# Optimization experiments

Measured on AMD Instinct MI355X. Metric: run time of the kernel, lower is better.

Reference implementation:

```python
import jax, jax.numpy as jnp
import numpy as np

N_EMBD = 1024
N_HEAD = 16
HEAD_SIZE = N_EMBD // N_HEAD  # 64

def setup_inputs() -> dict:
    key = jax.random.key(0)
    ks = jax.random.split(key, 6)
    B, T, C, H, S = 2, 2048, N_EMBD, N_HEAD, HEAD_SIZE
    sc = 1.0 / np.sqrt(C)
    x = jax.random.normal(ks[0], (B, T, C), dtype=jnp.float32)
    # stacked per-head projection weights (no bias), [H, C, S]
    Wq = jax.random.normal(ks[1], (H, C, S), dtype=jnp.float32) * sc
    Wk = jax.random.normal(ks[2], (H, C, S), dtype=jnp.float32) * sc
    Wv = jax.random.normal(ks[3], (H, C, S), dtype=jnp.float32) * sc
    Wp = jax.random.normal(ks[4], (C, C), dtype=jnp.float32) * sc
    bp = jax.random.normal(ks[5], (C,), dtype=jnp.float32) * 0.01
    return {"x": x, "Wq": Wq, "Wk": Wk, "Wv": Wv, "Wp": Wp, "bp": bp}

def reference(x, Wq, Wk, Wv, Wp, bp):
    # Eval-mode forward (dropout = identity), default non-flash path.
    B, T, C = x.shape
    H, _, S = Wq.shape
    q = jnp.einsum('btc,hcs->bhts', x, Wq)
    k = jnp.einsum('btc,hcs->bhts', x, Wk)
    v = jnp.einsum('btc,hcs->bhts', x, Wv)
    att = jnp.einsum('bhts,bhus->bhtu', q, k) * (1.0 / np.sqrt(S))
    causal = jnp.tril(jnp.ones((T, T), dtype=bool))
    att = jnp.where(causal[None, None], att, -jnp.inf)
    att = jax.nn.softmax(att, axis=-1)
    y = jnp.einsum('bhtu,bhus->bhts', att, v)
    # concat heads along feature dim (head-major), then output projection
    y = y.transpose(0, 2, 1, 3).reshape(B, T, H * S)
    return y @ Wp.T + bp
```

## Files before the change

### kernel.cpp

```cpp
#include <hip/hip_runtime.h>
#include <hip/hip_bf16.h>
#include <cmath>

typedef __attribute__((ext_vector_type(8))) short bf16x8;
typedef __attribute__((ext_vector_type(4))) float f32x4;
typedef __attribute__((ext_vector_type(16))) float f32x16;

__device__ __forceinline__ unsigned short f2bf(float f) {
    union { float f; unsigned int i; } c; c.f = f;
    unsigned int i = c.i;
    unsigned int r = i + 0x7FFF + ((i >> 16) & 1);
    return (unsigned short)(r >> 16);
}

__device__ __forceinline__ float fast_exp2(float x) {
    float r;
    asm("v_exp_f32 %0, %1" : "=v"(r) : "v"(x));
    return r;
}

__device__ __forceinline__ void gload_lds16(const unsigned short* g, unsigned short* l) {
    __builtin_amdgcn_global_load_lds((const __attribute__((address_space(1))) unsigned int*)g,
                                     (__attribute__((address_space(3))) unsigned int*)l, 16, 0, 0);
}

__global__ void k_cvt_all(const float* __restrict__ x, const float* __restrict__ Wp,
                          const float* __restrict__ Wq, const float* __restrict__ Wk,
                          const float* __restrict__ Wv,
                          unsigned short* __restrict__ x_bf, unsigned short* __restrict__ Wp_bf,
                          unsigned short* __restrict__ Wt) {
    __shared__ unsigned short lt[64][72];
    int bid = blockIdx.x;
    int t = threadIdx.x;
    if (bid < 5120) {
        const float* src = (bid < 4096) ? x : Wp;
        unsigned short* dst = (bid < 4096) ? x_bf : Wp_bf;
        int i = ((bid < 4096) ? bid : (bid - 4096)) * 256 + t;
        float4 v = reinterpret_cast<const float4*>(src)[i];
        ushort4 o;
        o.x = f2bf(v.x); o.y = f2bf(v.y); o.z = f2bf(v.z); o.w = f2bf(v.w);
        reinterpret_cast<ushort4*>(dst)[i] = o;
        return;
    }
    int sub = bid - 5120;
    int ct  = sub & 15;
    int h   = (sub >> 4) & 15;
    int sec = sub >> 8;
    const float* W = (sec == 0) ? Wq : ((sec == 1) ? Wk : Wv);
    float sc = (sec == 0) ? 0.1803368801f : 1.0f;
    #pragma unroll
    for (int q = 0; q < 4; q++) {
        int id = t + q * 256;
        int c  = id >> 4;
        int s4 = (id & 15) * 4;
        float4 v = *reinterpret_cast<const float4*>(&W[((size_t)(h * 1024) + (ct * 64 + c)) * 64 + s4]);
        lt[s4 + 0][c] = f2bf(v.x * sc);
        lt[s4 + 1][c] = f2bf(v.y * sc);
        lt[s4 + 2][c] = f2bf(v.z * sc);
        lt[s4 + 3][c] = f2bf(v.w * sc);
    }
    __syncthreads();
    #pragma unroll
    for (int q = 0; q < 2; q++) {
        int id = t + q * 256;
        int s  = id >> 3;
        int c8 = (id & 7) * 8;
        bf16x8 val = *reinterpret_cast<const bf16x8*>(&lt[s][c8]);
        int n = sec * 1024 + h * 64 + s;
        *reinterpret_cast<bf16x8*>(&Wt[(size_t)n * 1024 + ct * 64 + c8]) = val;
    }
}

__launch_bounds__(256, 3)
__global__ void k_gemm_qkv(const unsigned short* __restrict__ x_bf,
                           const unsigned short* __restrict__ Wt,
                           unsigned short* __restrict__ q_nat,
                           unsigned short* __restrict__ k_nat,
                           unsigned short* __restrict__ vT) {
    __shared__ unsigned short Asm[3][128][32];
    __shared__ unsigned short Bsm[3][128][32];
    const int K = 1024;
    int cpx = gridDim.x >> 3;
    int bid = (blockIdx.x & 7) * cpx + (blockIdx.x >> 3);
    bool isV = (bid >= 512);
    const unsigned short* A;
    const unsigned short* Bt;
    int m0, n0;
    if (!isV) {
        n0 = (bid & 15) << 7;
        m0 = (bid >> 4) << 7;
        A = x_bf; Bt = Wt;
    } else {
        int vb = bid - 512;
        n0 = (vb & 31) << 7;
        m0 = (vb >> 5) << 7;
        A = Wt + (size_t)2048 * 1024;
        Bt = x_bf;
    }
    int t = threadIdx.x;
    int lane = t & 63, w = t >> 6;
    int wr = w >> 1, wc = w & 1;
    int l15 = lane & 15, lg = lane >> 4;
    int srow = lane >> 2;
    int scol = ((lane & 3) ^ ((lane >> 3) & 3)) << 3;

    f32x4 acc[4][4];
    #pragma unroll
    for (int i = 0; i < 4; i++)
        #pragma unroll
        for (int j = 0; j < 4; j++) acc[i][j] = (f32x4){0.f, 0.f, 0.f, 0.f};

    auto STAGE = [&](int kt, int buf) {
        #pragma unroll
        for (int q = 0; q < 2; q++) {
            int rb = q * 64 + w * 16;
            int row = rb + srow;
            gload_lds16(&A[(size_t)(m0 + row) * K + kt + scol], &Asm[buf][rb][0]);
            gload_lds16(&Bt[(size_t)(n0 + row) * K + kt + scol], &Bsm[buf][rb][0]);
        }
    };

    const int NT = K >> 5;
    STAGE(0, 0);
    STAGE(32, 1);
    asm volatile("s_waitcnt vmcnt(4)" ::: "memory");
    __builtin_amdgcn_s_barrier();
    int cur = 0;

    for (int tt = 0; tt < NT; tt++) {
        bool more = (tt + 2 < NT);
        if (more) {
            int sbuf = cur + 2; if (sbuf >= 3) sbuf -= 3;
            STAGE((tt + 2) << 5, sbuf);
        }

        bf16x8 af[4], bfr[4];
        int xg = (l15 >> 1) & 3;
        #pragma unroll
        for (int mi = 0; mi < 4; mi++) {
            int row = wr * 64 + mi * 16 + l15;
            af[mi] = *reinterpret_cast<const bf16x8*>((const char*)&Asm[cur][row][0] + ((lg ^ xg) << 4));
        }
        #pragma unroll
        for (int nj = 0; nj < 4; nj++) {
            int row = wc * 64 + nj * 16 + l15;
            bfr[nj] = *reinterpret_cast<const bf16x8*>((const char*)&Bsm[cur][row][0] + ((lg ^ xg) << 4));
        }
        asm volatile("s_waitcnt lgkmcnt(0)" ::: "memory");
        __builtin_amdgcn_sched_barrier(0);
        __builtin_amdgcn_s_setprio(1);
        #pragma unroll
        for (int mi = 0; mi < 4; mi++)
            #pragma unroll
            for (int nj = 0; nj < 4; nj++)
                acc[mi][nj] = __builtin_amdgcn_mfma_f32_16x16x32_bf16(af[mi], bfr[nj], acc[mi][nj], 0, 0, 0);
        __builtin_amdgcn_s_setprio(0);

        if (more) {
            asm volatile("s_waitcnt vmcnt(4)" ::: "memory");
        } else {
            asm volatile("s_waitcnt vmcnt(0)" ::: "memory");
        }
        __builtin_amdgcn_s_barrier();
        cur = (cur == 2) ? 0 : cur + 1;
    }

    unsigned short* qkdst = nullptr;
    int noff = 0;
    if (!isV) { qkdst = (n0 < 1024) ? q_nat : k_nat; noff = (n0 < 1024) ? 0 : 1024; }
    #pragma unroll
    for (int mi = 0; mi < 4; mi++) {
        #pragma unroll
        for (int nj = 0; nj < 4; nj++) {
            #pragma unroll
            for (int r = 0; r < 4; r++) {
                int m = m0 + wr * 64 + mi * 16 + lg * 4 + r;
                int n = n0 + wc * 64 + nj * 16 + l15;
                float v = acc[mi][nj][r];
                if (!isV) {
                    qkdst[(size_t)m * 1024 + (n - noff)] = f2bf(v);
                } else {
                    int bb = n >> 11, ttn = n & 2047;
                    int hh = m >> 6, ss = m & 63;
                    vT[(((size_t)(bb * 16 + hh)) * 64 + ss) * 2048 + ttn] = f2bf(v);
                }
            }
        }
    }
}

__launch_bounds__(512, 4)
__global__ void k_attn(const unsigned short* __restrict__ q_nat,
                       const unsigned short* __restrict__ k_nat,
                       const unsigned short* __restrict__ vT,
                       unsigned short* __restrict__ y_bf) {
    __shared__ __align__(16) unsigned short SM[2][2][128][64];
    __shared__ float clB[128];
    const int T = 2048, H = 16;
    int bid = blockIdx.x;
    int bh = bid & 31;
    int g  = bid >> 5;
    int p  = (g < 8) ? (15 - g) : (g - 8);
    int h = bh & 15, b = bh >> 4;
    int t = threadIdx.x;
    int lane = t & 63, w = t >> 6;
    int pr = w >> 2, rg = w & 3;
    int l31 = lane & 31, hi = lane >> 5;
    int q0 = p << 7;
    int warp_q0 = q0 + rg * 32;
    int qg = warp_q0 + l31;

    const unsigned short* kbase = k_nat + (size_t)(b * T) * 1024 + h * 64;
    const unsigned short* vbase = vT + ((size_t)(b * H + h) * 64) * 2048;

    int sxor = ((lane & 7) ^ (lane >> 3)) << 3;

    auto STAGE = [&](int jt) {
        #pragma unroll
        for (int r = 0; r < 4; r++) {
            int rb = r * 32 + rg * 8;
            int grow = rb + (lane >> 3);
            gload_lds16(kbase + (size_t)(jt * 128 + grow) * 1024 + sxor, &SM[0][pr][rb][0]);
            gload_lds16(vbase + (size_t)(grow & 63) * 2048 + jt * 128 + (grow >> 6) * 64 + sxor,
                        &SM[1][pr][rb][0]);
        }
    };

    bf16x8 qf[4];
    #pragma unroll
    for (int tt = 0; tt < 4; tt++)
        qf[tt] = *reinterpret_cast<const bf16x8*>(
            q_nat + (size_t)(b * T + qg) * 1024 + h * 64 + tt * 16 + hi * 8);

    bf16x8 ones;
    #pragma unroll
    for (int z = 0; z < 8; z++) ones[z] = (short)0x3F80;

    f32x16 acc0, acc1, lacc;
    #pragma unroll
    for (int r = 0; r < 16; r++) { acc0[r] = 0.f; acc1[r] = 0.f; lacc[r] = 0.f; }

    if (pr == 0) STAGE(0);
    __syncthreads();

    for (int k = 0; k <= p; k++) {
        bool iCompute = (pr == (k & 1));
        if (!iCompute) {
            if (k + 1 <= p) STAGE(k + 1);
        } else {
            int rsw = (l31 & 7) << 4;
            #pragma unroll
            for (int jj = 0; jj < 2; jj++) {
                const char* kb = (const char*)&SM[0][pr][jj * 64][0];
                const char* vb = (const char*)&SM[1][pr][jj * 64][0];
                int j64 = 2 * k + jj;

                f32x16 s0, s1;
                #pragma unroll
                for (int r = 0; r < 16; r++) { s0[r] = 0.f; s1[r] = 0.f; }
                __builtin_amdgcn_s_setprio(1);
                #pragma unroll
                for (int tt = 0; tt < 4; tt++) {
                    int cb = (tt * 32 + hi * 16) ^ rsw;
                    bf16x8 kf0 = *reinterpret_cast<const bf16x8*>(kb + l31 * 128 + cb);
                    bf16x8 kf1 = *reinterpret_cast<const bf16x8*>(kb + (32 + l31) * 128 + cb);
                    s0 = __builtin_amdgcn_mfma_f32_32x32x16_bf16(kf0, qf[tt], s0, 0, 0, 0);
                    s1 = __builtin_amdgcn_mfma_f32_32x32x16_bf16(kf1, qf[tt], s1, 0, 0, 0);
                }
                __builtin_amdgcn_s_setprio(0);

                if (j64 * 64 + 63 > warp_q0) {
                    #pragma unroll
                    for (int r = 0; r < 16; r++) {
                        int kvr = (r & 3) + 8 * (r >> 2) + 4 * hi + j64 * 64;
                        if (kvr > qg) s0[r] = -INFINITY;
                        if (kvr + 32 > qg) s1[r] = -INFINITY;
                    }
                }

                #pragma unroll
                for (int r = 0; r < 16; r++) {
                    s0[r] = fast_exp2(s0[r]);
                    s1[r] = fast_exp2(s1[r]);
                }

                unsigned int c[16];
                #pragma unroll
                for (int i2 = 0; i2 < 8; i2++) {
                    asm("v_cvt_pk_bf16_f32 %0, %1, %2" : "=v"(c[i2]) : "v"(s0[2 * i2]), "v"(s0[2 * i2 + 1]));
                    asm("v_cvt_pk_bf16_f32 %0, %1, %2" : "=v"(c[8 + i2]) : "v"(s1[2 * i2]), "v"(s1[2 * i2 + 1]));
                }
                bf16x8 pa[4];
                #pragma unroll
                for (int ks = 0; ks < 4; ks++) {
                    unsigned int clo0 = c[ks * 4 + 0], clo1 = c[ks * 4 + 1];
                    unsigned int chi0 = c[ks * 4 + 2], chi1 = c[ks * 4 + 3];
                    unsigned int pl0 = (unsigned int)__shfl_xor((int)clo0, 32, 64);
                    unsigned int pl1 = (unsigned int)__shfl_xor((int)clo1, 32, 64);
                    unsigned int ph0 = (unsigned int)__shfl_xor((int)chi0, 32, 64);
                    unsigned int ph1 = (unsigned int)__shfl_xor((int)chi1, 32, 64);
                    union { unsigned int u[4]; bf16x8 v; } fr;
                    fr.u[0] = hi ? ph0 : clo0;
                    fr.u[1] = hi ? ph1 : clo1;
                    fr.u[2] = hi ? chi0 : pl0;
                    fr.u[3] = hi ? chi1 : pl1;
                    pa[ks] = fr.v;
                }

                __builtin_amdgcn_s_setprio(1);
                #pragma unroll
                for (int ks = 0; ks < 4; ks++) {
                    int cb = (ks * 32 + hi * 16) ^ rsw;
                    bf16x8 v0 = *reinterpret_cast<const bf16x8*>(vb + l31 * 128 + cb);
                    bf16x8 v1 = *reinterpret_cast<const bf16x8*>(vb + (32 + l31) * 128 + cb);
                    acc0 = __builtin_amdgcn_mfma_f32_32x32x16_bf16(pa[ks], v0, acc0, 0, 0, 0);
                    acc1 = __builtin_amdgcn_mfma_f32_32x32x16_bf16(pa[ks], v1, acc1, 0, 0, 0);
                    lacc = __builtin_amdgcn_mfma_f32_32x32x16_bf16(pa[ks], ones, lacc, 0, 0, 0);
                }
                __builtin_amdgcn_s_setprio(0);
            }
        }

        __syncthreads();
    }

    float* Ocomb = (float*)&SM[0][0][0][0];
    if (pr == 1) {
        #pragma unroll
        for (int r = 0; r < 16; r++) {
            int qr = (r & 3) + 8 * (r >> 2) + 4 * hi;
            int rr = rg * 32 + qr;
            Ocomb[rr * 64 + l31] = acc0[r];
            Ocomb[rr * 64 + 32 + l31] = acc1[r];
            if (l31 == 0) clB[rr] = lacc[r];
        }
    }
    __syncthreads();
    if (pr == 0) {
        #pragma unroll
        for (int r = 0; r < 16; r++) {
            int qr = (r & 3) + 8 * (r >> 2) + 4 * hi;
            int rr = rg * 32 + qr;
            float lt2 = lacc[r] + clB[rr];
            float dv = 1.0f / lt2;
            float o0 = acc0[r] + Ocomb[rr * 64 + l31];
            float o1 = acc1[r] + Ocomb[rr * 64 + 32 + l31];
            size_t row = (size_t)(b * T + q0 + rr) * 1024 + h * 64;
            y_bf[row + l31] = f2bf(o0 * dv);
            y_bf[row + 32 + l31] = f2bf(o1 * dv);
        }
    }
}

__launch_bounds__(256, 2)
__global__ void k_gemm_proj(const unsigned short* __restrict__ A,
                            const unsigned short* __restrict__ Bt,
                            float* __restrict__ out, const float* __restrict__ bp) {
    __shared__ unsigned short Asm[2][128][64];
    __shared__ unsigned short Bsm[2][64][64];
    const int K = 1024, nb = 16;
    int cpx = gridDim.x >> 3;
    int bid = (blockIdx.x & 7) * cpx + (blockIdx.x >> 3);
    int n0 = (bid % nb) << 6;
    int m0 = (bid / nb) << 7;
    int t = threadIdx.x;
    int lane = t & 63, w = t >> 6;
    int wr = w >> 1, wc = w & 1;
    int l15 = lane & 15, lg = lane >> 4;
    int sr = lane >> 3;
    int scol = ((lane & 7) ^ sr) << 3;

    f32x4 acc[4][2];
    #pragma unroll
    for (int i = 0; i < 4; i++)
        #pragma unroll
        for (int j = 0; j < 2; j++) acc[i][j] = (f32x4){0.f, 0.f, 0.f, 0.f};

    auto STAGE = [&](int kt, int buf) {
        #pragma unroll
        for (int q = 0; q < 4; q++) {
            int rb = q * 32 + w * 8;
            gload_lds16(&A[(size_t)(m0 + rb + sr) * K + kt + scol], &Asm[buf][rb][0]);
        }
        #pragma unroll
        for (int q = 0; q < 2; q++) {
            int rb = q * 32 + w * 8;
            gload_lds16(&Bt[(size_t)(n0 + rb + sr) * K + kt + scol], &Bsm[buf][rb][0]);
        }
    };

    const int NT = K >> 6;
    STAGE(0, 0);
    asm volatile("s_waitcnt vmcnt(0)" ::: "memory");
    __builtin_amdgcn_s_barrier();
    int cur = 0;

    for (int tt = 0; tt < NT; tt++) {
        if (tt + 1 < NT) STAGE((tt + 1) << 6, cur ^ 1);
        bf16x8 af[4][2], bfr[2][2];
        int x15 = (l15 & 7) << 3;
        #pragma unroll
        for (int mi = 0; mi < 4; mi++) {
            int row = wr * 64 + mi * 16 + l15;
            af[mi][0] = *reinterpret_cast<const bf16x8*>(&Asm[cur][row][(lg * 8) ^ x15]);
            af[mi][1] = *reinterpret_cast<const bf16x8*>(&Asm[cur][row][(32 + lg * 8) ^ x15]);
        }
        #pragma unroll
        for (int nj = 0; nj < 2; nj++) {
            int row = wc * 32 + nj * 16 + l15;
            bfr[nj][0] = *reinterpret_cast<const bf16x8*>(&Bsm[cur][row][(lg * 8) ^ x15]);
            bfr[nj][1] = *reinterpret_cast<const bf16x8*>(&Bsm[cur][row][(32 + lg * 8) ^ x15]);
        }
        asm volatile("s_waitcnt lgkmcnt(0)" ::: "memory");
        __builtin_amdgcn_sched_barrier(0);
        __builtin_amdgcn_s_setprio(1);
        #pragma unroll
        for (int mi = 0; mi < 4; mi++)
            #pragma unroll
            for (int nj = 0; nj < 2; nj++) {
                acc[mi][nj] = __builtin_amdgcn_mfma_f32_16x16x32_bf16(af[mi][0], bfr[nj][0], acc[mi][nj], 0, 0, 0);
                acc[mi][nj] = __builtin_amdgcn_mfma_f32_16x16x32_bf16(af[mi][1], bfr[nj][1], acc[mi][nj], 0, 0, 0);
            }
        __builtin_amdgcn_s_setprio(0);
        asm volatile("s_waitcnt vmcnt(0)" ::: "memory");
        __builtin_amdgcn_s_barrier();
        cur ^= 1;
    }

    #pragma unroll
    for (int mi = 0; mi < 4; mi++)
        #pragma unroll
        for (int nj = 0; nj < 2; nj++)
            #pragma unroll
            for (int r = 0; r < 4; r++) {
                int m = m0 + wr * 64 + mi * 16 + lg * 4 + r;
                int n = n0 + wc * 32 + nj * 16 + l15;
                out[(size_t)m * 1024 + n] = acc[mi][nj][r] + bp[n];
            }
}

extern "C" void kernel_launch(void* const* d_in, const int* in_sizes, int n_in,
                              void* d_out, int out_size, void* d_ws, size_t ws_size,
                              hipStream_t stream) {
    const float* x  = (const float*)d_in[0];
    const float* Wq = (const float*)d_in[1];
    const float* Wk = (const float*)d_in[2];
    const float* Wv = (const float*)d_in[3];
    const float* Wp = (const float*)d_in[4];
    const float* bp = (const float*)d_in[5];
    float* out = (float*)d_out;

    char* ws = (char*)d_ws;
    unsigned short* x_bf  = (unsigned short*)(ws);
    unsigned short* Wt    = (unsigned short*)(ws + ((size_t)8  << 20));
    unsigned short* Wp_bf = (unsigned short*)(ws + ((size_t)14 << 20));
    unsigned short* q_nat = (unsigned short*)(ws + ((size_t)16 << 20));
    unsigned short* k_nat = (unsigned short*)(ws + ((size_t)24 << 20));
    unsigned short* vT    = (unsigned short*)(ws + ((size_t)32 << 20));
    unsigned short* y_bf  = (unsigned short*)(ws + ((size_t)40 << 20));

    k_cvt_all<<<5888, 256, 0, stream>>>(x, Wp, Wq, Wk, Wv, x_bf, Wp_bf, Wt);
    k_gemm_qkv<<<768, 256, 0, stream>>>(x_bf, Wt, q_nat, k_nat, vT);
    k_attn<<<512, 512, 0, stream>>>(q_nat, k_nat, vT, y_bf);
    k_gemm_proj<<<512, 256, 0, stream>>>(y_bf, Wp_bf, out, bp);
}
```

Baseline: 101.2 us.

## Replace ping-pong warp groups with double-buffered all-warp prefetch in attention

Previously half the warps loaded the next K/V tile while the other half computed both 64-row halves of the current tile. Now every warp issues part of the prefetch into an alternate buffer, then each warp-group computes one 64-key half of the current tile, so all warps do MFMA work every iteration. The launch-bounds occupancy hint drops from 4 to 2 blocks, which gives the compiler more registers per thread but may lower occupancy. The shared layout is reinterpreted as two buffers, and the final combine that reuses SM is unchanged.

```diff
diff --git a/kernel.cpp b/kernel.cpp
--- a/kernel.cpp
+++ b/kernel.cpp
@@ -189,7 +189,7 @@
     }
 }
 
-__launch_bounds__(512, 4)
+__launch_bounds__(512, 2)
 __global__ void k_attn(const unsigned short* __restrict__ q_nat,
                        const unsigned short* __restrict__ k_nat,
                        const unsigned short* __restrict__ vT,
@@ -215,14 +215,15 @@
 
     int sxor = ((lane & 7) ^ (lane >> 3)) << 3;
 
-    auto STAGE = [&](int jt) {
-        #pragma unroll
-        for (int r = 0; r < 4; r++) {
-            int rb = r * 32 + rg * 8;
+    auto STAGE = [&](int jt, int buf) {
+        #pragma unroll
+        for (int q = 0; q < 2; q++) {
+            int rb = w * 16 + q * 8;
             int grow = rb + (lane >> 3);
-            gload_lds16(kbase + (size_t)(jt * 128 + grow) * 1024 + sxor, &SM[0][pr][rb][0]);
+            gload_lds16(kbase + (size_t)(jt * 128 + grow) * 1024 + sxor,
+                        (unsigned short*)&SM[buf][0][0][0] + rb * 64);
             gload_lds16(vbase + (size_t)(grow & 63) * 2048 + jt * 128 + (grow >> 6) * 64 + sxor,
-                        &SM[1][pr][rb][0]);
+                        (unsigned short*)&SM[buf][1][0][0] + rb * 64);
         }
     };
 
@@ -240,88 +241,84 @@
     #pragma unroll
     for (int r = 0; r < 16; r++) { acc0[r] = 0.f; acc1[r] = 0.f; lacc[r] = 0.f; }
 
-    if (pr == 0) STAGE(0);
+    STAGE(0, 0);
     __syncthreads();
+    int buf = 0;
 
     for (int k = 0; k <= p; k++) {
-        bool iCompute = (pr == (k & 1));
-        if (!iCompute) {
-            if (k + 1 <= p) STAGE(k + 1);
-        } else {
-            int rsw = (l31 & 7) << 4;
+        if (k < p) STAGE(k + 1, buf ^ 1);
+
+        const char* kb = (const char*)&SM[buf][0][pr * 64][0];
+        const char* vb = (const char*)&SM[buf][1][pr * 64][0];
+        int rsw = (l31 & 7) << 4;
+        int j64 = 2 * k + pr;
+
+        f32x16 s0, s1;
+        #pragma unroll
+        for (int r = 0; r < 16; r++) { s0[r] = 0.f; s1[r] = 0.f; }
+        __builtin_amdgcn_s_setprio(1);
+        #pragma unroll
+        for (int tt = 0; tt < 4; tt++) {
+            int cb = (tt * 32 + hi * 16) ^ rsw;
+            bf16x8 kf0 = *reinterpret_cast<const bf16x8*>(kb + l31 * 128 + cb);
+            bf16x8 kf1 = *reinterpret_cast<const bf16x8*>(kb + (32 + l31) * 128 + cb);
+            s0 = __builtin_amdgcn_mfma_f32_32x32x16_bf16(kf0, qf[tt], s0, 0, 0, 0);
+            s1 = __builtin_amdgcn_mfma_f32_32x32x16_bf16(kf1, qf[tt], s1, 0, 0, 0);
+        }
+        __builtin_amdgcn_s_setprio(0);
+
+        if (j64 * 64 + 63 > warp_q0) {
             #pragma unroll
-            for (int jj = 0; jj < 2; jj++) {
-                const char* kb = (const char*)&SM[0][pr][jj * 64][0];
-                const char* vb = (const char*)&SM[1][pr][jj * 64][0];
-                int j64 = 2 * k + jj;
-
-                f32x16 s0, s1;
-                #pragma unroll
-                for (int r = 0; r < 16; r++) { s0[r] = 0.f; s1[r] = 0.f; }
-                __builtin_amdgcn_s_setprio(1);
-                #pragma unroll
-                for (int tt = 0; tt < 4; tt++) {
-                    int cb = (tt * 32 + hi * 16) ^ rsw;
-                    bf16x8 kf0 = *reinterpret_cast<const bf16x8*>(kb + l31 * 128 + cb);
-                    bf16x8 kf1 = *reinterpret_cast<const bf16x8*>(kb + (32 + l31) * 128 + cb);
-                    s0 = __builtin_amdgcn_mfma_f32_32x32x16_bf16(kf0, qf[tt], s0, 0, 0, 0);
-                    s1 = __builtin_amdgcn_mfma_f32_32x32x16_bf16(kf1, qf[tt], s1, 0, 0, 0);
-                }
-                __builtin_amdgcn_s_setprio(0);
-
-                if (j64 * 64 + 63 > warp_q0) {
-                    #pragma unroll
-                    for (int r = 0; r < 16; r++) {
-                        int kvr = (r & 3) + 8 * (r >> 2) + 4 * hi + j64 * 64;
-                        if (kvr > qg) s0[r] = -INFINITY;
-                        if (kvr + 32 > qg) s1[r] = -INFINITY;
-                    }
-                }
-
-                #pragma unroll
-                for (int r = 0; r < 16; r++) {
-                    s0[r] = fast_exp2(s0[r]);
-                    s1[r] = fast_exp2(s1[r]);
-                }
-
-                unsigned int c[16];
-                #pragma unroll
-                for (int i2 = 0; i2 < 8; i2++) {
-                    asm("v_cvt_pk_bf16_f32 %0, %1, %2" : "=v"(c[i2]) : "v"(s0[2 * i2]), "v"(s0[2 * i2 + 1]));
-                    asm("v_cvt_pk_bf16_f32 %0, %1, %2" : "=v"(c[8 + i2]) : "v"(s1[2 * i2]), "v"(s1[2 * i2 + 1]));
-                }
-                bf16x8 pa[4];
-                #pragma unroll
-                for (int ks = 0; ks < 4; ks++) {
-                    unsigned int clo0 = c[ks * 4 + 0], clo1 = c[ks * 4 + 1];
-                    unsigned int chi0 = c[ks * 4 + 2], chi1 = c[ks * 4 + 3];
-                    unsigned int pl0 = (unsigned int)__shfl_xor((int)clo0, 32, 64);
-                    unsigned int pl1 = (unsigned int)__shfl_xor((int)clo1, 32, 64);
-                    unsigned int ph0 = (unsigned int)__shfl_xor((int)chi0, 32, 64);
-                    unsigned int ph1 = (unsigned int)__shfl_xor((int)chi1, 32, 64);
-                    union { unsigned int u[4]; bf16x8 v; } fr;
-                    fr.u[0] = hi ? ph0 : clo0;
-                    fr.u[1] = hi ? ph1 : clo1;
-                    fr.u[2] = hi ? chi0 : pl0;
-                    fr.u[3] = hi ? chi1 : pl1;
-                    pa[ks] = fr.v;
-                }
-
-                __builtin_amdgcn_s_setprio(1);
-                #pragma unroll
-                for (int ks = 0; ks < 4; ks++) {
-                    int cb = (ks * 32 + hi * 16) ^ rsw;
-                    bf16x8 v0 = *reinterpret_cast<const bf16x8*>(vb + l31 * 128 + cb);
-                    bf16x8 v1 = *reinterpret_cast<const bf16x8*>(vb + (32 + l31) * 128 + cb);
-                    acc0 = __builtin_amdgcn_mfma_f32_32x32x16_bf16(pa[ks], v0, acc0, 0, 0, 0);
-                    acc1 = __builtin_amdgcn_mfma_f32_32x32x16_bf16(pa[ks], v1, acc1, 0, 0, 0);
-                    lacc = __builtin_amdgcn_mfma_f32_32x32x16_bf16(pa[ks], ones, lacc, 0, 0, 0);
-                }
-                __builtin_amdgcn_s_setprio(0);
+            for (int r = 0; r < 16; r++) {
+                int kvr = (r & 3) + 8 * (r >> 2) + 4 * hi + j64 * 64;
+                if (kvr > qg) s0[r] = -INFINITY;
+                if (kvr + 32 > qg) s1[r] = -INFINITY;
             }
         }
 
+        #pragma unroll
+        for (int r = 0; r < 16; r++) {
+            s0[r] = fast_exp2(s0[r]);
+            s1[r] = fast_exp2(s1[r]);
+        }
+
+        unsigned int c[16];
+        #pragma unroll
+        for (int i2 = 0; i2 < 8; i2++) {
+            asm("v_cvt_pk_bf16_f32 %0, %1, %2" : "=v"(c[i2]) : "v"(s0[2 * i2]), "v"(s0[2 * i2 + 1]));
+            asm("v_cvt_pk_bf16_f32 %0, %1, %2" : "=v"(c[8 + i2]) : "v"(s1[2 * i2]), "v"(s1[2 * i2 + 1]));
+        }
+        bf16x8 pa[4];
+        #pragma unroll
+        for (int ks = 0; ks < 4; ks++) {
+            unsigned int clo0 = c[ks * 4 + 0], clo1 = c[ks * 4 + 1];
+            unsigned int chi0 = c[ks * 4 + 2], chi1 = c[ks * 4 + 3];
+            unsigned int pl0 = (unsigned int)__shfl_xor((int)clo0, 32, 64);
+            unsigned int pl1 = (unsigned int)__shfl_xor((int)clo1, 32, 64);
+            unsigned int ph0 = (unsigned int)__shfl_xor((int)chi0, 32, 64);
+            unsigned int ph1 = (unsigned int)__shfl_xor((int)chi1, 32, 64);
+            union { unsigned int u[4]; bf16x8 v; } fr;
+            fr.u[0] = hi ? ph0 : clo0;
+            fr.u[1] = hi ? ph1 : clo1;
+            fr.u[2] = hi ? chi0 : pl0;
+            fr.u[3] = hi ? chi1 : pl1;
+            pa[ks] = fr.v;
+        }
+
+        __builtin_amdgcn_s_setprio(1);
+        #pragma unroll
+        for (int ks = 0; ks < 4; ks++) {
+            int cb = (ks * 32 + hi * 16) ^ rsw;
+            bf16x8 v0 = *reinterpret_cast<const bf16x8*>(vb + l31 * 128 + cb);
+            bf16x8 v1 = *reinterpret_cast<const bf16x8*>(vb + (32 + l31) * 128 + cb);
+            acc0 = __builtin_amdgcn_mfma_f32_32x32x16_bf16(pa[ks], v0, acc0, 0, 0, 0);
+            acc1 = __builtin_amdgcn_mfma_f32_32x32x16_bf16(pa[ks], v1, acc1, 0, 0, 0);
+            lacc = __builtin_amdgcn_mfma_f32_32x32x16_bf16(pa[ks], ones, lacc, 0, 0, 0);
+        }
+        __builtin_amdgcn_s_setprio(0);
+
         __syncthreads();
+        buf ^= 1;
     }
 
     float* Ocomb = (float*)&SM[0][0][0][0];
```

Measured after the change: 107.2 us. +6.0%, slower.
